# Kernel optimization log

Measured on AMD Instinct MI355X. Metric: run time of the kernel, lower is better.

Reference implementation:

```python
import jax, jax.numpy as jnp
import numpy as np

B, T, H, DI, DO = 512, 512, 100, 101, 2
DT_OVER_TAU = 0.1  # dt=1, tau=10


def retanh(x):
    return jnp.maximum(jnp.tanh(x), 0.0)


def setup_inputs() -> dict:
    key = jax.random.key(0)
    k0, k1, k2, k3 = jax.random.split(key, 4)
    inp = jax.random.normal(k0, (B, T, DI), jnp.float32)
    noise = jax.random.normal(k1, (B, T, H), jnp.float32) * 0.1
    W_x_ah = (jax.random.normal(k2, (H, DI), jnp.float32) / np.sqrt(DI)).astype(jnp.float32)
    b_ah = jnp.zeros((H,), jnp.float32)
    # orthogonalized recurrent weights (svd with unit singular values), as in __init__
    A = np.random.default_rng(0).standard_normal((H, H))
    u, _, vT = np.linalg.svd(A)
    W_h_ah = jnp.asarray(u @ vT, jnp.float32)
    # original inits W_h_y to zeros; use small random so output is nontrivial
    W_h_y = jax.random.normal(k3, (DO, H), jnp.float32) * 0.1
    ah0 = jnp.zeros((H,), jnp.float32)
    return {"input": inp, "noise": noise, "W_x_ah": W_x_ah, "b_ah": b_ah,
            "W_h_ah": W_h_ah, "W_h_y": W_h_y, "ah0": ah0}


def reference(input, noise, W_x_ah, b_ah, W_h_ah, W_h_y, ah0):
    # precompute input projection as one batched GEMM: [B,T,H]
    xp = jnp.einsum('bti,hi->bth', input, W_x_ah) + b_ah
    ah_init = jnp.broadcast_to(ah0, (input.shape[0], ah0.shape[0]))
    h_init = retanh(ah_init)

    def step(carry, xs):
        ah, h = carry
        xp_t, nz_t = xs
        ah = ah + DT_OVER_TAU * (-ah + h @ W_h_ah.T + xp_t)
        h = retanh(ah) + nz_t
        return (ah, h), h

    _, hstore = jax.lax.scan(step, (ah_init, h_init),
                             (xp.transpose(1, 0, 2), noise.transpose(1, 0, 2)))
    hstore = hstore.transpose(1, 0, 2)  # [B,T,H]
    output = hstore @ W_h_y.T  # [B,T,DO]
    return output, hstore
```

## Files before the change

### kernel.cpp

```cpp
#include <hip/hip_runtime.h>
#include <hip/hip_bf16.h>

#define BB 512
#define TT 512
#define HH 100
#define DI 101
#define DOUT 2
#define BT (BB * TT)

typedef float f4 __attribute__((ext_vector_type(4)));

__global__ __launch_bounds__(128, 2) void k_inproj(
    const float* __restrict__ in, const float* __restrict__ Wx,
    const float* __restrict__ bias, float* __restrict__ xp) {
  const int t = threadIdx.x;
  const int p = t >> 1;
  const int kh = t & 1;
  const int c0 = p;
  const int c1 = p + 64;
  const bool c1ok = (c1 < HH);

  __shared__ __align__(16) float Atile[64 * 104];

  float4 wx0[13], wx1[13];
  {
    const float* w0 = Wx + (size_t)c0 * DI + kh * 52;
    const float* w1 = Wx + (size_t)(c1ok ? c1 : 0) * DI + kh * 52;
    const int nk = kh ? 49 : 52;
#pragma unroll
    for (int j = 0; j < 13; ++j) {
      float a0 = (4 * j + 0 < nk) ? w0[4 * j + 0] : 0.f;
      float a1 = (4 * j + 1 < nk) ? w0[4 * j + 1] : 0.f;
      float a2 = (4 * j + 2 < nk) ? w0[4 * j + 2] : 0.f;
      float a3 = (4 * j + 3 < nk) ? w0[4 * j + 3] : 0.f;
      wx0[j] = make_float4(a0, a1, a2, a3);
      float b0v = (4 * j + 0 < nk) ? w1[4 * j + 0] : 0.f;
      float b1v = (4 * j + 1 < nk) ? w1[4 * j + 1] : 0.f;
      float b2v = (4 * j + 2 < nk) ? w1[4 * j + 2] : 0.f;
      float b3v = (4 * j + 3 < nk) ? w1[4 * j + 3] : 0.f;
      wx1[j] = make_float4(b0v, b1v, b2v, b3v);
    }
  }
  const float bs0 = bias[c0];
  const float bs1 = c1ok ? bias[c1] : 0.f;

  const int row0 = blockIdx.x * 64;

  {
    const float* rp = in + (size_t)(row0 + p) * DI + kh * 52;
    float* dst = Atile + p * 104 + kh * 52;
#pragma unroll
    for (int j = 0; j < 52; ++j) {
      float v;
      if (kh == 0) v = rp[j];
      else        v = (52 + j < DI) ? rp[j] : 0.f;
      dst[j] = v;
    }
  }
  __syncthreads();

#pragma unroll 2
  for (int r = 0; r < 64; ++r) {
    const float4* a4 = (const float4*)(Atile + r * 104 + kh * 52);
    float4 s0 = make_float4(0.f, 0.f, 0.f, 0.f);
    float4 s1 = make_float4(0.f, 0.f, 0.f, 0.f);
#pragma unroll
    for (int j = 0; j < 13; ++j) {
      float4 av = a4[j];
      s0.x = fmaf(av.x, wx0[j].x, s0.x);
      s0.y = fmaf(av.y, wx0[j].y, s0.y);
      s0.z = fmaf(av.z, wx0[j].z, s0.z);
      s0.w = fmaf(av.w, wx0[j].w, s0.w);
      s1.x = fmaf(av.x, wx1[j].x, s1.x);
      s1.y = fmaf(av.y, wx1[j].y, s1.y);
      s1.z = fmaf(av.z, wx1[j].z, s1.z);
      s1.w = fmaf(av.w, wx1[j].w, s1.w);
    }
    float p0 = (s0.x + s0.y) + (s0.z + s0.w);
    float p1 = (s1.x + s1.y) + (s1.z + s1.w);
    p0 += __shfl_xor(p0, 1, 64);
    p1 += __shfl_xor(p1, 1, 64);
    if (kh == 0) {
      float* xr = xp + (size_t)(row0 + r) * HH;
      xr[c0] = p0 + bs0;
      if (c1ok) xr[c1] = p1 + bs1;
    }
  }
}

__global__ __launch_bounds__(64, 1) void k_scan(
    const float* __restrict__ noise, const float* __restrict__ Wh,
    const float* __restrict__ ah0, const float* __restrict__ Wy,
    float* __restrict__ out, float* hstore ) {
  const int b = blockIdx.x;
  const int l = threadIdx.x;
  const bool act = (l < 50);
  const int s0 = act ? 2 * l : 0;

  __shared__ __align__(16) float h_lds[HH];

  f4 w0[25], w1[25];
  {
    const f4* r0 = (const f4*)(Wh + (size_t)s0 * HH);
    const f4* r1 = (const f4*)(Wh + (size_t)(s0 + 1) * HH);
#pragma unroll
    for (int j = 0; j < 25; ++j) {
      w0[j] = r0[j];
      w1[j] = r1[j];
    }
  }
  float wy00 = 0.f, wy01 = 0.f, wy10 = 0.f, wy11 = 0.f;
  if (act) {
    float2 wa = *(const float2*)(Wy + s0);
    float2 wb = *(const float2*)(Wy + HH + s0);
    wy00 = wa.x; wy01 = wa.y; wy10 = wb.x; wy11 = wb.y;
  }

  float ahx = 0.f, ahy = 0.f;
  if (act) {
    float2 a = *(const float2*)(ah0 + s0);
    ahx = a.x; ahy = a.y;
  }
  {
    float e0 = __expf(-2.f * ahx);
    float e1 = __expf(-2.f * ahy);
    float h0 = (ahx > 0.f) ? (1.f - e0) * __builtin_amdgcn_rcpf(1.f + e0) : 0.f;
    float h1 = (ahy > 0.f) ? (1.f - e1) * __builtin_amdgcn_rcpf(1.f + e1) : 0.f;
    if (act) *(float2*)&h_lds[s0] = make_float2(h0, h1);
  }

  const float* xp_base = hstore;
  const size_t bbase = (size_t)b * TT * HH;
  float2* out2 = (float2*)out;

  float2 xpA = make_float2(0.f, 0.f), nzA = xpA;
  float2 xpB = xpA, nzB = xpA, xpC = xpA, nzC = xpA, xpD = xpA, nzD = xpA;
  if (act) {
    xpA = *(const float2*)(xp_base + bbase + (size_t)0 * HH + s0);
    nzA = *(const float2*)(noise + bbase + (size_t)0 * HH + s0);
    xpB = *(const float2*)(xp_base + bbase + (size_t)1 * HH + s0);
    nzB = *(const float2*)(noise + bbase + (size_t)1 * HH + s0);
    xpC = *(const float2*)(xp_base + bbase + (size_t)2 * HH + s0);
    nzC = *(const float2*)(noise + bbase + (size_t)2 * HH + s0);
    xpD = *(const float2*)(xp_base + bbase + (size_t)3 * HH + s0);
    nzD = *(const float2*)(noise + bbase + (size_t)3 * HH + s0);
  }

#define STEP(XP, NZ, tc)                                                      \
  {                                                                           \
    const int tpf = (tc) + 4;                                                 \
    float2 nxp = make_float2(0.f, 0.f), nnz = nxp;                            \
    if (act && tpf < TT) {                                                    \
      nxp = *(const float2*)(xp_base + bbase + (size_t)tpf * HH + s0);        \
      nnz = *(const float2*)(noise + bbase + (size_t)tpf * HH + s0);          \
    }                                                                         \
    const f4* h4 = (const f4*)h_lds;                                          \
    f4 acc0 = {0.f, 0.f, 0.f, 0.f};                                           \
    f4 acc1 = {0.f, 0.f, 0.f, 0.f};                                           \
    _Pragma("unroll") for (int j = 0; j < 25; ++j) {                          \
      f4 hv = h4[j];                      \
      acc0 = __builtin_elementwise_fma(w0[j], hv, acc0);                      \
      acc1 = __builtin_elementwise_fma(w1[j], hv, acc1);                      \
    }                                                                         \
    float d0 = (acc0.x + acc0.y) + (acc0.z + acc0.w);                         \
    float d1 = (acc1.x + acc1.y) + (acc1.z + acc1.w);                         \
    ahx = fmaf(0.1f, (d0 + XP.x) - ahx, ahx);                                 \
    ahy = fmaf(0.1f, (d1 + XP.y) - ahy, ahy);                                 \
    float e0 = __expf(-2.f * ahx);                                            \
    float e1 = __expf(-2.f * ahy);                                            \
    float h0 = (ahx > 0.f) ? (1.f - e0) * __builtin_amdgcn_rcpf(1.f + e0)     \
                           : 0.f;                                             \
    float h1 = (ahy > 0.f) ? (1.f - e1) * __builtin_amdgcn_rcpf(1.f + e1)     \
                           : 0.f;                                             \
    h0 += NZ.x;                                                               \
    h1 += NZ.y;                                                               \
             \
    if (act) {                                                                \
      *(float2*)&h_lds[s0] = make_float2(h0, h1);                             \
      *(float2*)(hstore + bbase + (size_t)(tc)*HH + s0) =                     \
          make_float2(h0, h1);                                                \
    }                                                                         \
               \
    float po0 = act ? fmaf(h0, wy00, h1 * wy01) : 0.f;                        \
    float po1 = act ? fmaf(h0, wy10, h1 * wy11) : 0.f;                        \
    po0 += __shfl_xor(po0, 1, 64);                                            \
    po1 += __shfl_xor(po1, 1, 64);                                            \
    po0 += __shfl_xor(po0, 2, 64);                                            \
    po1 += __shfl_xor(po1, 2, 64);                                            \
    po0 += __shfl_xor(po0, 4, 64);                                            \
    po1 += __shfl_xor(po1, 4, 64);                                            \
    po0 += __shfl_xor(po0, 8, 64);                                            \
    po1 += __shfl_xor(po1, 8, 64);                                            \
    po0 += __shfl_xor(po0, 16, 64);                                           \
    po1 += __shfl_xor(po1, 16, 64);                                           \
    po0 += __shfl_xor(po0, 32, 64);                                           \
    po1 += __shfl_xor(po1, 32, 64);                                           \
    if (l == 0) out2[(size_t)b * TT + (tc)] = make_float2(po0, po1);          \
    XP = nxp;                                                                 \
    NZ = nnz;                                                                 \
  }

#pragma unroll 1
  for (int tc = 0; tc < TT; tc += 4) {
    STEP(xpA, nzA, tc);
    STEP(xpB, nzB, tc + 1);
    STEP(xpC, nzC, tc + 2);
    STEP(xpD, nzD, tc + 3);
  }
#undef STEP
}

extern "C" void kernel_launch(void* const* d_in, const int* in_sizes, int n_in,
                              void* d_out, int out_size, void* d_ws,
                              size_t ws_size, hipStream_t stream) {
  const float* input = (const float*)d_in[0];
  const float* noise = (const float*)d_in[1];
  const float* W_x = (const float*)d_in[2];
  const float* b_ah = (const float*)d_in[3];
  const float* W_h = (const float*)d_in[4];
  const float* W_y = (const float*)d_in[5];
  const float* ah0 = (const float*)d_in[6];

  float* out = (float*)d_out;
  float* hstore = out + (size_t)BB * TT * DOUT;

  k_inproj<<<BT / 64, 128, 0, stream>>>(input, W_x, b_ah, hstore);

  k_scan<<<BB, 64, 0, stream>>>(noise, W_h, ah0, W_y, out, hstore);
}
```

Measured before the change: 727.7 us.

## Pad Wx in prep kernel, coalesce input tile loads, split scan accumulators

Adds a small prep kernel that pads W_x rows to 104 floats in workspace, so the input-projection kernel can load weights as aligned float4 vectors. It also changes the input-tile load from per-thread strided scalar reads to coalesced float4 reads scattered into LDS. In the scan kernel, the 25-term dot product now uses two even/odd accumulator chains to shorten the FMA dependency chain, and empty asm statements pin the W_h registers. The cost is an extra kernel launch plus integer div/mod work in the LDS scatter.

```diff
diff --git a/kernel.cpp b/kernel.cpp
--- a/kernel.cpp
+++ b/kernel.cpp
@@ -10,8 +10,17 @@
 
 typedef float f4 __attribute__((ext_vector_type(4)));
 
+__global__ void k_prep(const float* __restrict__ Wx, float* __restrict__ WxP) {
+  const int t = threadIdx.x;
+  for (int idx = t; idx < HH * 104; idx += 256) {
+    const int r = idx / 104;
+    const int c = idx - r * 104;
+    WxP[idx] = (c < DI) ? Wx[r * DI + c] : 0.f;
+  }
+}
+
 __global__ __launch_bounds__(128, 2) void k_inproj(
-    const float* __restrict__ in, const float* __restrict__ Wx,
+    const float* __restrict__ in, const float* __restrict__ WxP,
     const float* __restrict__ bias, float* __restrict__ xp) {
   const int t = threadIdx.x;
   const int p = t >> 1;
@@ -22,23 +31,14 @@
 
   __shared__ __align__(16) float Atile[64 * 104];
 
-  float4 wx0[13], wx1[13];
-  {
-    const float* w0 = Wx + (size_t)c0 * DI + kh * 52;
-    const float* w1 = Wx + (size_t)(c1ok ? c1 : 0) * DI + kh * 52;
-    const int nk = kh ? 49 : 52;
+  f4 wx0[13], wx1[13];
+  {
+    const f4* w0p = (const f4*)(WxP + (size_t)c0 * 104 + kh * 52);
+    const f4* w1p = (const f4*)(WxP + (size_t)(c1ok ? c1 : 0) * 104 + kh * 52);
 #pragma unroll
     for (int j = 0; j < 13; ++j) {
-      float a0 = (4 * j + 0 < nk) ? w0[4 * j + 0] : 0.f;
-      float a1 = (4 * j + 1 < nk) ? w0[4 * j + 1] : 0.f;
-      float a2 = (4 * j + 2 < nk) ? w0[4 * j + 2] : 0.f;
-      float a3 = (4 * j + 3 < nk) ? w0[4 * j + 3] : 0.f;
-      wx0[j] = make_float4(a0, a1, a2, a3);
-      float b0v = (4 * j + 0 < nk) ? w1[4 * j + 0] : 0.f;
-      float b1v = (4 * j + 1 < nk) ? w1[4 * j + 1] : 0.f;
-      float b2v = (4 * j + 2 < nk) ? w1[4 * j + 2] : 0.f;
-      float b3v = (4 * j + 3 < nk) ? w1[4 * j + 3] : 0.f;
-      wx1[j] = make_float4(b0v, b1v, b2v, b3v);
+      wx0[j] = w0p[j];
+      wx1[j] = w1p[j];
     }
   }
   const float bs0 = bias[c0];
@@ -47,34 +47,40 @@
   const int row0 = blockIdx.x * 64;
 
   {
-    const float* rp = in + (size_t)(row0 + p) * DI + kh * 52;
-    float* dst = Atile + p * 104 + kh * 52;
-#pragma unroll
-    for (int j = 0; j < 52; ++j) {
-      float v;
-      if (kh == 0) v = rp[j];
-      else        v = (52 + j < DI) ? rp[j] : 0.f;
-      dst[j] = v;
+    const f4* src = (const f4*)(in + (size_t)row0 * DI);
+#pragma unroll
+    for (int j = 0; j < 13; ++j) {
+      const int Q = j * 128 + t;
+      if (Q < 1616) {
+        f4 v = src[Q];
+        const int m = 4 * Q;
+#pragma unroll
+        for (int kcomp = 0; kcomp < 4; ++kcomp) {
+          const int mi = m + kcomp;
+          const int r = mi / 101;
+          const int c = mi - r * 101;
+          Atile[r * 104 + c] = v[kcomp];
+        }
+      }
+    }
+    if (t < 64) {
+      Atile[t * 104 + 101] = 0.f;
+      Atile[t * 104 + 102] = 0.f;
+      Atile[t * 104 + 103] = 0.f;
     }
   }
   __syncthreads();
 
 #pragma unroll 2
   for (int r = 0; r < 64; ++r) {
-    const float4* a4 = (const float4*)(Atile + r * 104 + kh * 52);
-    float4 s0 = make_float4(0.f, 0.f, 0.f, 0.f);
-    float4 s1 = make_float4(0.f, 0.f, 0.f, 0.f);
+    const f4* a4 = (const f4*)(Atile + r * 104 + kh * 52);
+    f4 s0 = {0.f, 0.f, 0.f, 0.f};
+    f4 s1 = {0.f, 0.f, 0.f, 0.f};
 #pragma unroll
     for (int j = 0; j < 13; ++j) {
-      float4 av = a4[j];
-      s0.x = fmaf(av.x, wx0[j].x, s0.x);
-      s0.y = fmaf(av.y, wx0[j].y, s0.y);
-      s0.z = fmaf(av.z, wx0[j].z, s0.z);
-      s0.w = fmaf(av.w, wx0[j].w, s0.w);
-      s1.x = fmaf(av.x, wx1[j].x, s1.x);
-      s1.y = fmaf(av.y, wx1[j].y, s1.y);
-      s1.z = fmaf(av.z, wx1[j].z, s1.z);
-      s1.w = fmaf(av.w, wx1[j].w, s1.w);
+      f4 av = a4[j];
+      s0 = __builtin_elementwise_fma(av, wx0[j], s0);
+      s1 = __builtin_elementwise_fma(av, wx1[j], s1);
     }
     float p0 = (s0.x + s0.y) + (s0.z + s0.w);
     float p1 = (s1.x + s1.y) + (s1.z + s1.w);
@@ -107,6 +113,10 @@
     for (int j = 0; j < 25; ++j) {
       w0[j] = r0[j];
       w1[j] = r1[j];
+    }
+#pragma unroll
+    for (int j = 0; j < 25; ++j) {
+      asm volatile("" : "+v"(w0[j]), "+v"(w1[j]));
     }
   }
   float wy00 = 0.f, wy01 = 0.f, wy10 = 0.f, wy11 = 0.f;
@@ -155,13 +165,23 @@
       nnz = *(const float2*)(noise + bbase + (size_t)tpf * HH + s0);          \
     }                                                                         \
     const f4* h4 = (const f4*)h_lds;                                          \
-    f4 acc0 = {0.f, 0.f, 0.f, 0.f};                                           \
-    f4 acc1 = {0.f, 0.f, 0.f, 0.f};                                           \
-    _Pragma("unroll") for (int j = 0; j < 25; ++j) {                          \
-      f4 hv = h4[j];                      \
-      acc0 = __builtin_elementwise_fma(w0[j], hv, acc0);                      \
-      acc1 = __builtin_elementwise_fma(w1[j], hv, acc1);                      \
-    }                                                                         \
+    f4 a0e = {0.f, 0.f, 0.f, 0.f}, a0o = a0e;                                 \
+    f4 a1e = a0e, a1o = a0e;                                                  \
+    _Pragma("unroll") for (int j = 0; j < 24; j += 2) {                       \
+      f4 hvE = h4[j];                     \
+      f4 hvO = h4[j + 1];                                                     \
+      a0e = __builtin_elementwise_fma(w0[j], hvE, a0e);                       \
+      a1e = __builtin_elementwise_fma(w1[j], hvE, a1e);                       \
+      a0o = __builtin_elementwise_fma(w0[j + 1], hvO, a0o);                   \
+      a1o = __builtin_elementwise_fma(w1[j + 1], hvO, a1o);                   \
+    }                                                                         \
+    {                                                                         \
+      f4 hvL = h4[24];                                                        \
+      a0e = __builtin_elementwise_fma(w0[24], hvL, a0e);                      \
+      a1e = __builtin_elementwise_fma(w1[24], hvL, a1e);                      \
+    }                                                                         \
+    f4 acc0 = a0e + a0o;                                                      \
+    f4 acc1 = a1e + a1o;                                                      \
     float d0 = (acc0.x + acc0.y) + (acc0.z + acc0.w);                         \
     float d1 = (acc1.x + acc1.y) + (acc1.z + acc1.w);                         \
     ahx = fmaf(0.1f, (d0 + XP.x) - ahx, ahx);                                 \
@@ -223,8 +243,11 @@
 
   float* out = (float*)d_out;
   float* hstore = out + (size_t)BB * TT * DOUT;
-
-  k_inproj<<<BT / 64, 128, 0, stream>>>(input, W_x, b_ah, hstore);
+  float* WxP = (float*)d_ws;
+
+  k_prep<<<1, 256, 0, stream>>>(W_x, WxP);
+
+  k_inproj<<<BT / 64, 128, 0, stream>>>(input, WxP, b_ah, hstore);
 
   k_scan<<<BB, 64, 0, stream>>>(noise, W_h, ah0, W_y, out, hstore);
 }
```

Result: slower. 757.9 us (+4.2%).
